# Kernel tuning notes

Hardware: AMD Instinct MI355X
Metric: run time of the kernel (lower is better)

The kernel has to match this reference:

```python
import jax, jax.numpy as jnp
import numpy as np
import math

B, S, D = 2, 1024, 1024
H = 16
HD = D // H
E = 8
DFF = 4096
EPS = 1e-5


def _ln(x, g, b):
    m = jnp.mean(x, axis=-1, keepdims=True)
    v = jnp.mean((x - m) ** 2, axis=-1, keepdims=True)
    return (x - m) / jnp.sqrt(v + EPS) * g + b


def setup_inputs() -> dict:
    key = jax.random.key(0)
    ks = jax.random.split(key, 16)
    s = 0.02
    inp = {
        'src': jax.random.normal(ks[0], (B, S, D), jnp.float32),
        'qw': jax.random.normal(ks[1], (D, D), jnp.float32) * s,
        'kw': jax.random.normal(ks[2], (D, D), jnp.float32) * s,
        'vw': jax.random.normal(ks[3], (D, D), jnp.float32) * s,
        'ow': jax.random.normal(ks[4], (D, D), jnp.float32) * s,
        'gate_w': jax.random.normal(ks[5], (D, D), jnp.float32) * s,
        'gate_b': jax.random.normal(ks[6], (D,), jnp.float32) * s,
        'scale_w': jax.random.normal(ks[7], (H, HD), jnp.float32) * s,
        'n1_g': jnp.ones((D,), jnp.float32),
        'n1_b': jnp.zeros((D,), jnp.float32),
        'n2_g': jnp.ones((D,), jnp.float32),
        'n2_b': jnp.zeros((D,), jnp.float32),
        'moe_gate_w': jax.random.normal(ks[8], (D, E), jnp.float32) * s,
        'moe_gate_b': jnp.zeros((E,), jnp.float32),
        'w1': jax.random.normal(ks[9], (E, D, DFF), jnp.float32) * s,
        'b1': jnp.zeros((E, DFF), jnp.float32),
        'ln_g': jnp.ones((E, DFF), jnp.float32),
        'ln_b': jnp.zeros((E, DFF), jnp.float32),
        'w2': jax.random.normal(ks[10], (E, DFF, D), jnp.float32) * s,
        'b2': jnp.zeros((E, D), jnp.float32),
        'res_scale': jnp.ones((E,), jnp.float32),
    }
    return inp


def _forward(src, qw, kw, vw, ow, gate_w, gate_b, scale_w, n1_g, n1_b, n2_g, n2_b,
             moe_gate_w, moe_gate_b, w1, b1, ln_g, ln_b, w2, b2, res_scale):
    # ---- MemoAttention (non-flash path, eval: no dropout, no mask) ----
    q = (src @ qw).reshape(B, S, H, HD).transpose(0, 2, 1, 3)  # [B,H,S,HD]
    k = (src @ kw).reshape(B, S, H, HD).transpose(0, 2, 1, 3)
    v = (src @ vw).reshape(B, S, H, HD).transpose(0, 2, 1, 3)
    scores = jnp.einsum('bhqd,bhkd->bhqk', q, k) / math.sqrt(HD)
    # dynamic per-(head,query) scale gate
    scale = jax.nn.sigmoid(jnp.einsum('bhsd,hd->bhs', q, scale_w)) * 2.0
    scores = scores * scale[..., None]
    attn = jax.nn.softmax(scores, axis=-1)
    out = jnp.einsum('bhqk,bhkd->bhqd', attn, v)
    out = out.transpose(0, 2, 1, 3).reshape(B, S, D)
    gate = jax.nn.sigmoid(out @ gate_w + gate_b)
    attn_out = (out * gate) @ ow

    x = _ln(src + attn_out, n1_g, n1_b)

    # ---- MoE FFN (top-2 routing; eval: no gate noise; capacity never exceeded) ----
    xf = x.reshape(-1, D)                      # [T, D]
    T = xf.shape[0]
    logits = xf @ moe_gate_w + moe_gate_b      # [T, E]
    top_v, top_i = jax.lax.top_k(logits, 2)
    # NB: original sums BOTH top-k softmax weights per token (== 1.0), and the
    wsum = jnp.sum(jax.nn.softmax(top_v, axis=-1), axis=-1)   # [T] (== 1)
    e_sel = jnp.max(top_i, axis=-1)                           # [T]
    # dense per-expert FFN on all tokens, then per-token select (masked compute)
    h = jnp.einsum('td,edf->etf', xf, w1) + b1[:, None, :]    # [E,T,DFF]
    h = _ln(h, ln_g[:, None, :], ln_b[:, None, :])
    h = jax.nn.gelu(h, approximate=False)                     # torch nn.GELU (erf)
    y = jnp.einsum('etf,efd->etd', h, w2) + b2[:, None, :]    # [E,T,D]
    y = y * res_scale[:, None, None] + xf[None]
    sel = jnp.take_along_axis(y, e_sel[None, :, None], axis=0)[0]  # [T,D]
    moe_out = (sel * wsum[:, None]).reshape(B, S, D)

    return _ln(x + moe_out, n2_g, n2_b)


def reference(src, qw, kw, vw, ow, gate_w, gate_b, scale_w, n1_g, n1_b, n2_g, n2_b,
              moe_gate_w, moe_gate_b, w1, b1, ln_g, ln_b, w2, b2, res_scale):
    return _forward(src, qw, kw, vw, ow, gate_w, gate_b, scale_w, n1_g, n1_b,
                    n2_g, n2_b, moe_gate_w, moe_gate_b, w1, b1, ln_g, ln_b,
                    w2, b2, res_scale)
```

## Files before the change

kernel.cpp:

```cpp
#include <hip/hip_runtime.h>
#include <math.h>

#define TOK    2048
#define DMODEL 1024
#define NHEAD  16
#define HDIM   64
#define NEXP   8
#define DFFN   4096

typedef unsigned short u16;
typedef __attribute__((ext_vector_type(8))) short short8;
typedef __attribute__((ext_vector_type(4))) float floatx4;

__device__ __forceinline__ float sigmoidf_(float x) { return 1.f / (1.f + expf(-x)); }

__device__ __forceinline__ u16 f2bf(float f) {
  union { float f; unsigned u; } v; v.f = f;
  unsigned r = v.u + 0x7FFFu + ((v.u >> 16) & 1u);
  return (u16)(r >> 16);
}
__device__ __forceinline__ float bf2f(u16 h) {
  union { unsigned u; float f; } v; v.u = ((unsigned)h) << 16; return v.f;
}

__device__ __forceinline__ void gload16(const void* g, void* l) {
  __builtin_amdgcn_global_load_lds((const __attribute__((address_space(1))) void*)g,
                                   (__attribute__((address_space(3))) void*)l, 16, 0, 0);
}

__device__ __forceinline__ float blockReduceSum256(float val) {
  __shared__ float ws_[4];
  #pragma unroll
  for (int off = 32; off; off >>= 1) val += __shfl_down(val, off);
  int lane = threadIdx.x & 63, w = threadIdx.x >> 6;
  if (lane == 0) ws_[w] = val;
  __syncthreads();
  float r = ws_[0] + ws_[1] + ws_[2] + ws_[3];
  __syncthreads();
  return r;
}

__global__ __launch_bounds__(256) void split_kernel(
    const float* __restrict__ X, u16* __restrict__ Hi, u16* __restrict__ Lo) {
  const int i = blockIdx.x * 256 + threadIdx.x;
  const float4 v = ((const float4*)X)[i];
  const float f[4] = {v.x, v.y, v.z, v.w};
  union { u16 s[4]; uint2 u; } h, l;
  #pragma unroll
  for (int j = 0; j < 4; ++j) {
    h.s[j] = f2bf(f[j]);
    l.s[j] = f2bf(f[j] - bf2f(h.s[j]));
  }
  ((uint2*)Hi)[i] = h.u;
  ((uint2*)Lo)[i] = l.u;
}

template<bool LO>
__global__ __launch_bounds__(256) void wt_conv_kernel(
    const float* __restrict__ W, u16* __restrict__ Whi, u16* __restrict__ Wlo,
    int K, int N) {
  const size_t z = blockIdx.z;
  W   += z * (size_t)K * N;
  Whi += z * (size_t)K * N;
  if (LO) Wlo += z * (size_t)K * N;
  __shared__ float tile[32][33];
  const int n0 = blockIdx.x * 32, k0 = blockIdx.y * 32;
  const int r = threadIdx.x >> 3, c4 = (threadIdx.x & 7) * 4;
  const float4 v = *(const float4*)&W[(size_t)(k0 + r) * N + n0 + c4];
  tile[r][c4+0] = v.x; tile[r][c4+1] = v.y; tile[r][c4+2] = v.z; tile[r][c4+3] = v.w;
  __syncthreads();
  union { u16 s[4]; uint2 u; } h, l;
  #pragma unroll
  for (int j = 0; j < 4; ++j) {
    const float f = tile[c4 + j][r];
    h.s[j] = f2bf(f);
    if (LO) l.s[j] = f2bf(f - bf2f(h.s[j]));
  }
  *(uint2*)&Whi[(size_t)(n0 + r) * K + k0 + c4] = h.u;
  if (LO) *(uint2*)&Wlo[(size_t)(n0 + r) * K + k0 + c4] = l.u;
}

__global__ __launch_bounds__(256) void wt3_conv_kernel(
    const float* __restrict__ Q, const float* __restrict__ Kw,
    const float* __restrict__ V, u16* __restrict__ Whi, u16* __restrict__ Wlo) {
  const int zz = blockIdx.z >> 5;
  const float* W = (zz == 0) ? Q : (zz == 1) ? Kw : V;
  u16* Whi_ = Whi + (size_t)zz * DMODEL * DMODEL;
  u16* Wlo_ = Wlo + (size_t)zz * DMODEL * DMODEL;
  __shared__ float tile[32][33];
  const int n0 = blockIdx.x * 32, k0 = (blockIdx.z & 31) * 32;
  const int r = threadIdx.x >> 3, c4 = (threadIdx.x & 7) * 4;
  const float4 v = *(const float4*)&W[(size_t)(k0 + r) * DMODEL + n0 + c4];
  tile[r][c4+0] = v.x; tile[r][c4+1] = v.y; tile[r][c4+2] = v.z; tile[r][c4+3] = v.w;
  __syncthreads();
  union { u16 s[4]; uint2 u; } h, l;
  #pragma unroll
  for (int j = 0; j < 4; ++j) {
    const float f = tile[c4 + j][r];
    h.s[j] = f2bf(f);
    l.s[j] = f2bf(f - bf2f(h.s[j]));
  }
  *(uint2*)&Whi_[(size_t)(n0 + r) * DMODEL + k0 + c4] = h.u;
  *(uint2*)&Wlo_[(size_t)(n0 + r) * DMODEL + k0 + c4] = l.u;
}

template<int EPI, int TN>
__global__ __launch_bounds__(256, TN == 64 ? 3 : 2) void gemm_split_kernel(
    const u16* __restrict__ Ahi, const u16* __restrict__ Alo,
    const u16* __restrict__ Whi, const u16* __restrict__ Wlo,
    const float* __restrict__ bias, const float* __restrict__ mul,
    float* __restrict__ Cf, u16* __restrict__ Chi, u16* __restrict__ Clo,
    u16* __restrict__ Vth, u16* __restrict__ Vtl,
    int M, int N, int K) {
  constexpr int NF = TN / 32;
  __shared__ u16 Ah[128*64], Al[128*64], Bh[TN*64], Bl[TN*64];
  const int tid = threadIdx.x;
  const int lane = tid & 63, wave = tid >> 6;
  const int row0 = blockIdx.y * 128, col0 = blockIdx.x * TN;
  const int wm = (wave & 1) * 64, wn = (wave >> 1) * (TN / 2);
  const int mr = tid >> 3;
  const int ksrc = (tid & 7) ^ ((tid >> 3) & 7);
  const floatx4 zero = {0.f, 0.f, 0.f, 0.f};
  floatx4 acc[4][NF];
  #pragma unroll
  for (int i = 0; i < 4; ++i)
    #pragma unroll
    for (int j = 0; j < NF; ++j) acc[i][j] = zero;

  for (int k0 = 0; k0 < K; k0 += 64) {
    __syncthreads();
    #pragma unroll
    for (int p = 0; p < 4; ++p) {
      const size_t ga = (size_t)(row0 + p * 32 + mr) * K + (k0 + ksrc * 8);
      const size_t off = (size_t)(p * 256 + wave * 64) * 16;
      gload16(Ahi + ga, (char*)Ah + off);
      gload16(Alo + ga, (char*)Al + off);
    }
    #pragma unroll
    for (int p = 0; p < NF; ++p) {
      const size_t gb = (size_t)(col0 + p * 32 + mr) * K + (k0 + ksrc * 8);
      const size_t off = (size_t)(p * 256 + wave * 64) * 16;
      gload16(Whi + gb, (char*)Bh + off);
      gload16(Wlo + gb, (char*)Bl + off);
    }
    __syncthreads();
    #pragma unroll
    for (int kk = 0; kk < 2; ++kk) {
      short8 ah[4], al[4], bh[NF], bl[NF];
      #pragma unroll
      for (int i = 0; i < 4; ++i) {
        const int ml = wm + i * 16 + (lane & 15);
        const int cm = (kk * 4 + (lane >> 4)) ^ (ml & 7);
        ah[i] = *(const short8*)&Ah[ml * 64 + cm * 8];
        al[i] = *(const short8*)&Al[ml * 64 + cm * 8];
      }
      #pragma unroll
      for (int j = 0; j < NF; ++j) {
        const int nl = wn + j * 16 + (lane & 15);
        const int cn = (kk * 4 + (lane >> 4)) ^ (nl & 7);
        bh[j] = *(const short8*)&Bh[nl * 64 + cn * 8];
        bl[j] = *(const short8*)&Bl[nl * 64 + cn * 8];
      }
      #pragma unroll
      for (int i = 0; i < 4; ++i)
        #pragma unroll
        for (int j = 0; j < NF; ++j) {
          acc[i][j] = __builtin_amdgcn_mfma_f32_16x16x32_bf16(ah[i], bh[j], acc[i][j], 0, 0, 0);
          acc[i][j] = __builtin_amdgcn_mfma_f32_16x16x32_bf16(al[i], bh[j], acc[i][j], 0, 0, 0);
          acc[i][j] = __builtin_amdgcn_mfma_f32_16x16x32_bf16(ah[i], bl[j], acc[i][j], 0, 0, 0);
        }
    }
  }
  const int cl = lane & 15, quad = lane >> 4;
  if (EPI == 2 && col0 >= 2048) {
    #pragma unroll
    for (int i = 0; i < 4; ++i)
      #pragma unroll
      for (int j = 0; j < NF; ++j) {
        const int dg = col0 + wn + j * 16 + cl - 2048;
        const int bh_ = dg >> 6, d = dg & 63;
        const int row = row0 + wm + i * 16 + quad * 4;
        const int b = row >> 10, t0 = row & 1023;
        union { u16 s[4]; uint2 u; } hh, ll;
        #pragma unroll
        for (int r = 0; r < 4; ++r) {
          const float v = acc[i][j][r];
          hh.s[r] = f2bf(v);
          ll.s[r] = f2bf(v - bf2f(hh.s[r]));
        }
        const size_t base = ((size_t)(b * 16 + bh_) * 64 + d) * 1024 + t0;
        *(uint2*)&Vth[base] = hh.u;
        *(uint2*)&Vtl[base] = ll.u;
      }
    return;
  }
  #pragma unroll
  for (int i = 0; i < 4; ++i)
    #pragma unroll
    for (int j = 0; j < NF; ++j) {
      const int col = col0 + wn + j * 16 + cl;
      #pragma unroll
      for (int r = 0; r < 4; ++r) {
        const int row = row0 + wm + i * 16 + quad * 4 + r;
        const float v = acc[i][j][r];
        if (EPI == 0) {
          Cf[(size_t)row * N + col] = v;
        } else if (EPI == 1) {
          const float s = sigmoidf_(v + bias[col]);
          const float g = s * mul[(size_t)row * N + col];
          const u16 hh = f2bf(g);
          Chi[(size_t)row * N + col] = hh;
          Clo[(size_t)row * N + col] = f2bf(g - bf2f(hh));
        } else {
          const u16 hh = f2bf(v);
          Chi[(size_t)row * N + col] = hh;
          Clo[(size_t)row * N + col] = f2bf(v - bf2f(hh));
        }
      }
    }
}

template<int EPI, int TN>
__global__ __launch_bounds__(256, TN == 64 ? 4 : 3) void gemm_moe_kernel(
    const u16* __restrict__ A, const u16* __restrict__ Wt,
    const float* __restrict__ bias,
    const int* __restrict__ perm, const int* __restrict__ offs,
    const int* __restrict__ counts,
    u16* __restrict__ Hout, float* __restrict__ P0, float* __restrict__ P1,
    int N, int K, int e_base) {
  constexpr int NF = TN / 32;
  const int z = blockIdx.z;
  const int ez = (EPI == 0) ? z : (z & 3);
  const int ks = (EPI == 0) ? 0 : (z >> 2);
  const int e = e_base + ez;
  const int ne = counts[e];
  const int tm = blockIdx.y;
  if (tm * 128 >= ne) return;
  const int kbeg = (EPI == 0) ? 0 : ks * (K >> 1);
  const int kend = (EPI == 0) ? K : kbeg + (K >> 1);
  __shared__ u16 As_[128*64], Bs_[TN*64];
  __shared__ int toks[128];
  const int tid = threadIdx.x;
  if (tid < 128) {
    const int idx = tm * 128 + tid;
    toks[tid] = perm[offs[e] + (idx < ne ? idx : 0)];
  }
  __syncthreads();
  const int lane = tid & 63, wave = tid >> 6;
  const int wm = (wave & 1) * 64, wn = (wave >> 1) * (TN / 2);
  const int mr = tid >> 3;
  const int ksrc = (tid & 7) ^ ((tid >> 3) & 7);
  size_t abase[4];
  #pragma unroll
  for (int p = 0; p < 4; ++p) abase[p] = (size_t)toks[p * 32 + mr] * K;
  const u16* We = Wt + (size_t)ez * N * K;
  const int col0 = blockIdx.x * TN;
  const floatx4 zero = {0.f, 0.f, 0.f, 0.f};
  floatx4 acc[4][NF];
  #pragma unroll
  for (int i = 0; i < 4; ++i)
    #pragma unroll
    for (int j = 0; j < NF; ++j) acc[i][j] = zero;

  for (int k0 = kbeg; k0 < kend; k0 += 64) {
    __syncthreads();
    #pragma unroll
    for (int p = 0; p < 4; ++p) {
      const size_t off = (size_t)(p * 256 + wave * 64) * 16;
      gload16(A + abase[p] + (k0 + ksrc * 8), (char*)As_ + off);
    }
    #pragma unroll
    for (int p = 0; p < NF; ++p) {
      const size_t off = (size_t)(p * 256 + wave * 64) * 16;
      gload16(We + (size_t)(col0 + p * 32 + mr) * K + (k0 + ksrc * 8), (char*)Bs_ + off);
    }
    __syncthreads();
    #pragma unroll
    for (int kk = 0; kk < 2; ++kk) {
      short8 a[4], b[NF];
      #pragma unroll
      for (int i = 0; i < 4; ++i) {
        const int ml = wm + i * 16 + (lane & 15);
        const int cm = (kk * 4 + (lane >> 4)) ^ (ml & 7);
        a[i] = *(const short8*)&As_[ml * 64 + cm * 8];
      }
      #pragma unroll
      for (int j = 0; j < NF; ++j) {
        const int nl = wn + j * 16 + (lane & 15);
        const int cn = (kk * 4 + (lane >> 4)) ^ (nl & 7);
        b[j] = *(const short8*)&Bs_[nl * 64 + cn * 8];
      }
      #pragma unroll
      for (int i = 0; i < 4; ++i)
        #pragma unroll
        for (int j = 0; j < NF; ++j)
          acc[i][j] = __builtin_amdgcn_mfma_f32_16x16x32_bf16(a[i], b[j], acc[i][j], 0, 0, 0);
    }
  }
  const int cl = lane & 15, quad = lane >> 4;
  float* Pp = (EPI == 1) ? (ks ? P1 : P0) : nullptr;
  #pragma unroll
  for (int i = 0; i < 4; ++i)
    #pragma unroll
    for (int j = 0; j < NF; ++j) {
      const int col = col0 + wn + j * 16 + cl;
      #pragma unroll
      for (int r = 0; r < 4; ++r) {
        const int rl = wm + i * 16 + quad * 4 + r;
        if (tm * 128 + rl < ne) {
          const int tok = toks[rl];
          if (EPI == 0)
            Hout[(size_t)tok * N + col] = f2bf(acc[i][j][r] + bias[(size_t)e * N + col]);
          else
            Pp[(size_t)tok * N + col] = acc[i][j][r];
        }
      }
    }
}

__global__ __launch_bounds__(256, 2) void attn_mfma_kernel(
    const u16* __restrict__ QKh, const u16* __restrict__ QKl,
    const u16* __restrict__ Vth, const u16* __restrict__ Vtl,
    const float* __restrict__ scale_w,
    float* __restrict__ AOf, u16* __restrict__ AOh, u16* __restrict__ AOl) {
  const int qt = blockIdx.x, h = blockIdx.y, b = blockIdx.z;
  __shared__ u16 Kh[64*64], Kl[64*64], Vh[64*64], Vl[64*64];
  __shared__ u16 Ph[4][16*72], Pl[4][16*72];
  const int tid = threadIdx.x, lane = tid & 63, wave = tid >> 6;
  const int i15 = lane & 15, quad = lane >> 4;
  const floatx4 zero = {0.f, 0.f, 0.f, 0.f};

  short8 qh[2], ql[2];
  const size_t qrow = ((size_t)b * 1024 + qt * 64 + wave * 16 + i15) * 3072 + h * 64;
  #pragma unroll
  for (int kk = 0; kk < 2; ++kk) {
    qh[kk] = *(const short8*)&QKh[qrow + kk * 32 + quad * 8];
    ql[kk] = *(const short8*)&QKl[qrow + kk * 32 + quad * 8];
  }
  float dot = 0.f;
  #pragma unroll
  for (int kk = 0; kk < 2; ++kk)
    #pragma unroll
    for (int j = 0; j < 8; ++j) {
      const float sw = scale_w[h * 64 + kk * 32 + quad * 8 + j];
      dot += (bf2f((u16)qh[kk][j]) + bf2f((u16)ql[kk][j])) * sw;
    }
  dot += __shfl_xor(dot, 16);
  dot += __shfl_xor(dot, 32);
  const float g = 2.f * sigmoidf_(dot) * 0.125f;
  float stot[4];
  #pragma unroll
  for (int r = 0; r < 4; ++r) stot[r] = __shfl(g, (lane >> 4) * 4 + r);

  float m_r[4], l_r[4];
  floatx4 Of[4];
  #pragma unroll
  for (int r = 0; r < 4; ++r) { m_r[r] = -1e30f; l_r[r] = 0.f; }
  #pragma unroll
  for (int f = 0; f < 4; ++f) Of[f] = zero;
  u16* PhW = Ph[wave];
  u16* PlW = Pl[wave];

  const int sr = tid >> 3, sc = ((tid & 7) ^ ((tid >> 3) & 7)) * 8;
  for (int kt = 0; kt < 16; ++kt) {
    __syncthreads();
    #pragma unroll
    for (int p = 0; p < 2; ++p) {
      const int row = p * 32 + sr;
      const size_t off = (size_t)(p * 256 + wave * 64) * 16;
      const size_t kg = ((size_t)b * 1024 + kt * 64 + row) * 3072 + 1024 + h * 64 + sc;
      gload16(QKh + kg, (char*)Kh + off);
      gload16(QKl + kg, (char*)Kl + off);
      const size_t vg = ((size_t)(b * 16 + h) * 64 + row) * 1024 + kt * 64 + sc;
      gload16(Vth + vg, (char*)Vh + off);
      gload16(Vtl + vg, (char*)Vl + off);
    }
    __syncthreads();
    float pm[4][4];
    #pragma unroll
    for (int jn = 0; jn < 4; ++jn) {
      floatx4 a = zero;
      #pragma unroll
      for (int kk = 0; kk < 2; ++kk) {
        const int n = jn * 16 + i15;
        const int ch = ((kk * 4 + quad) ^ (n & 7)) * 8;
        const short8 bh = *(const short8*)&Kh[n * 64 + ch];
        const short8 bl = *(const short8*)&Kl[n * 64 + ch];
        a = __builtin_amdgcn_mfma_f32_16x16x32_bf16(qh[kk], bh, a, 0, 0, 0);
        a = __builtin_amdgcn_mfma_f32_16x16x32_bf16(ql[kk], bh, a, 0, 0, 0);
        a = __builtin_amdgcn_mfma_f32_16x16x32_bf16(qh[kk], bl, a, 0, 0, 0);
      }
      #pragma unroll
      for (int r = 0; r < 4; ++r) pm[jn][r] = a[r] * stot[r];
    }
    float alpha[4];
    #pragma unroll
    for (int r = 0; r < 4; ++r) {
      float mx = fmaxf(fmaxf(pm[0][r], pm[1][r]), fmaxf(pm[2][r], pm[3][r]));
      mx = fmaxf(mx, __shfl_xor(mx, 1));
      mx = fmaxf(mx, __shfl_xor(mx, 2));
      mx = fmaxf(mx, __shfl_xor(mx, 4));
      mx = fmaxf(mx, __shfl_xor(mx, 8));
      const float mn = fmaxf(m_r[r], mx);
      alpha[r] = expf(m_r[r] - mn);
      m_r[r] = mn;
      float rs = 0.f;
      #pragma unroll
      for (int jn = 0; jn < 4; ++jn) { pm[jn][r] = expf(pm[jn][r] - mn); rs += pm[jn][r]; }
      rs += __shfl_xor(rs, 1);
      rs += __shfl_xor(rs, 2);
      rs += __shfl_xor(rs, 4);
      rs += __shfl_xor(rs, 8);
      l_r[r] = l_r[r] * alpha[r] + rs;
    }
    #pragma unroll
    for (int f = 0; f < 4; ++f)
      #pragma unroll
      for (int r = 0; r < 4; ++r) Of[f][r] *= alpha[r];
    #pragma unroll
    for (int jn = 0; jn < 4; ++jn)
      #pragma unroll
      for (int r = 0; r < 4; ++r) {
        const int a = (quad * 4 + r) * 72 + jn * 16 + i15;
        const u16 hh = f2bf(pm[jn][r]);
        PhW[a] = hh;
        PlW[a] = f2bf(pm[jn][r] - bf2f(hh));
      }
    #pragma unroll
    for (int kk = 0; kk < 2; ++kk) {
      const short8 pah = *(const short8*)&PhW[i15 * 72 + kk * 32 + quad * 8];
      const short8 pal = *(const short8*)&PlW[i15 * 72 + kk * 32 + quad * 8];
      #pragma unroll
      for (int f = 0; f < 4; ++f) {
        const int d = f * 16 + i15;
        const int ch = ((kk * 4 + quad) ^ (d & 7)) * 8;
        const short8 vbh = *(const short8*)&Vh[d * 64 + ch];
        const short8 vbl = *(const short8*)&Vl[d * 64 + ch];
        Of[f] = __builtin_amdgcn_mfma_f32_16x16x32_bf16(pah, vbh, Of[f], 0, 0, 0);
        Of[f] = __builtin_amdgcn_mfma_f32_16x16x32_bf16(pal, vbh, Of[f], 0, 0, 0);
        Of[f] = __builtin_amdgcn_mfma_f32_16x16x32_bf16(pah, vbl, Of[f], 0, 0, 0);
      }
    }
  }
  float inv[4];
  #pragma unroll
  for (int r = 0; r < 4; ++r) inv[r] = 1.f / l_r[r];
  #pragma unroll
  for (int f = 0; f < 4; ++f)
    #pragma unroll
    for (int r = 0; r < 4; ++r) {
      const size_t row = (size_t)b * 1024 + qt * 64 + wave * 16 + quad * 4 + r;
      const int col = h * 64 + f * 16 + i15;
      const float val = Of[f][r] * inv[r];
      AOf[row * 1024 + col] = val;
      const u16 hh = f2bf(val);
      AOh[row * 1024 + col] = hh;
      AOl[row * 1024 + col] = f2bf(val - bf2f(hh));
    }
}

template<bool BF>
__global__ __launch_bounds__(256) void ln_add_kernel(
    const float* __restrict__ A, const float* __restrict__ Bp,
    const float* __restrict__ g, const float* __restrict__ beta,
    float* __restrict__ outf, u16* __restrict__ outh) {
  int t = blockIdx.x, tid = threadIdx.x;
  const float* a = A + (size_t)t * DMODEL;
  const float* b = Bp + (size_t)t * DMODEL;
  float v[4]; float s = 0.f;
  #pragma unroll
  for (int i = 0; i < 4; ++i) { int d = tid + i*256; v[i] = a[d] + b[d]; s += v[i]; }
  s = blockReduceSum256(s);
  float mean = s * (1.f/1024.f);
  float q = 0.f;
  #pragma unroll
  for (int i = 0; i < 4; ++i) { float df = v[i]-mean; q += df*df; }
  q = blockReduceSum256(q);
  float rstd = rsqrtf(q*(1.f/1024.f) + 1e-5f);
  #pragma unroll
  for (int i = 0; i < 4; ++i) {
    int d = tid + i*256;
    float val = (v[i]-mean)*rstd*g[d] + beta[d];
    outf[(size_t)t*DMODEL + d] = val;
    if (BF) outh[(size_t)t*DMODEL + d] = f2bf(val);
  }
}

__global__ __launch_bounds__(256) void ln_final_kernel(
    const float* __restrict__ X, const float* __restrict__ P0,
    const float* __restrict__ P1, const float* __restrict__ B2,
    const float* __restrict__ rsv, const int* __restrict__ e_sel,
    const float* __restrict__ g, const float* __restrict__ beta,
    float* __restrict__ out) {
  int t = blockIdx.x, tid = threadIdx.x;
  const int e = e_sel[t];
  const float rse = rsv[e];
  const float* b2e = B2 + (size_t)e * DMODEL;
  float v[4]; float s = 0.f;
  #pragma unroll
  for (int i = 0; i < 4; ++i) {
    int d = tid + i*256;
    const size_t idx = (size_t)t * DMODEL + d;
    const float xv = X[idx];
    const float yv = (P0[idx] + P1[idx] + b2e[d]) * rse + xv;
    v[i] = xv + yv;
    s += v[i];
  }
  s = blockReduceSum256(s);
  float mean = s * (1.f/1024.f);
  float q = 0.f;
  #pragma unroll
  for (int i = 0; i < 4; ++i) { float df = v[i]-mean; q += df*df; }
  q = blockReduceSum256(q);
  float rstd = rsqrtf(q*(1.f/1024.f) + 1e-5f);
  #pragma unroll
  for (int i = 0; i < 4; ++i) {
    int d = tid + i*256;
    out[(size_t)t*DMODEL + d] = (v[i]-mean)*rstd*g[d] + beta[d];
  }
}

__global__ __launch_bounds__(256) void moe_gate_kernel(
    const float* __restrict__ X, const float* __restrict__ gw,
    const float* __restrict__ gb, int* __restrict__ e_sel) {
  int wave = threadIdx.x >> 6, lane = threadIdx.x & 63;
  int token = blockIdx.x * 4 + wave;
  const float* x = X + (size_t)token * DMODEL;
  float acc[NEXP] = {};
  for (int d = lane; d < DMODEL; d += 64) {
    float xv = x[d];
    const float* gr = gw + (size_t)d * NEXP;
    #pragma unroll
    for (int e = 0; e < NEXP; ++e) acc[e] += xv * gr[e];
  }
  #pragma unroll
  for (int e = 0; e < NEXP; ++e) {
    #pragma unroll
    for (int off = 32; off; off >>= 1) acc[e] += __shfl_down(acc[e], off);
  }
  if (lane == 0) {
    float lg[NEXP];
    #pragma unroll
    for (int e = 0; e < NEXP; ++e) lg[e] = acc[e] + gb[e];
    int i1 = 0;
    for (int e = 1; e < NEXP; ++e) if (lg[e] > lg[i1]) i1 = e;
    int i2 = -1;
    for (int e = 0; e < NEXP; ++e) {
      if (e == i1) continue;
      if (i2 < 0 || lg[e] > lg[i2]) i2 = e;
    }
    e_sel[token] = (i1 > i2) ? i1 : i2;
  }
}

__global__ __launch_bounds__(256) void moe_group_kernel(
    const int* __restrict__ e_sel, int* __restrict__ perm,
    int* __restrict__ g_offs, int* __restrict__ g_counts) {
  __shared__ int cnt[NEXP], offs[NEXP], cur[NEXP];
  int tid = threadIdx.x;
  if (tid < NEXP) cnt[tid] = 0;
  __syncthreads();
  for (int t = tid; t < TOK; t += 256) atomicAdd(&cnt[e_sel[t]], 1);
  __syncthreads();
  if (tid == 0) {
    int run = 0;
    for (int e = 0; e < NEXP; ++e) { offs[e] = run; cur[e] = run; run += cnt[e]; }
  }
  __syncthreads();
  if (tid < NEXP) { g_offs[tid] = offs[tid]; g_counts[tid] = cnt[tid]; }
  for (int t = tid; t < TOK; t += 256) {
    int pos = atomicAdd(&cur[e_sel[t]], 1);
    perm[pos] = t;
  }
}

__global__ __launch_bounds__(256) void moe_ln_gelu_kernel(
    u16* __restrict__ H, const float* __restrict__ ln_g,
    const float* __restrict__ ln_b, const int* __restrict__ e_sel) {
  int t = blockIdx.x, tid = threadIdx.x;
  int e = e_sel[t];
  u16* h = H + (size_t)t * DFFN;
  float v[16]; float s = 0.f;
  #pragma unroll
  for (int i = 0; i < 16; ++i) { v[i] = bf2f(h[tid + i*256]); s += v[i]; }
  s = blockReduceSum256(s);
  float mean = s * (1.f/4096.f);
  float q = 0.f;
  #pragma unroll
  for (int i = 0; i < 16; ++i) { float df = v[i]-mean; q += df*df; }
  q = blockReduceSum256(q);
  float rstd = rsqrtf(q*(1.f/4096.f) + 1e-5f);
  const float* gg = ln_g + (size_t)e * DFFN;
  const float* bb = ln_b + (size_t)e * DFFN;
  #pragma unroll
  for (int i = 0; i < 16; ++i) {
    int d = tid + i*256;
    float x = (v[i]-mean)*rstd*gg[d] + bb[d];
    h[d] = f2bf(0.5f * x * (1.f + erff(x * 0.7071067811865475f)));
  }
}

extern "C" void kernel_launch(void* const* d_in, const int* in_sizes, int n_in,
                              void* d_out, int out_size, void* d_ws, size_t ws_size,
                              hipStream_t stream) {
  (void)in_sizes; (void)n_in; (void)out_size; (void)ws_size;
  const float* src    = (const float*)d_in[0];
  const float* qw     = (const float*)d_in[1];
  const float* kw     = (const float*)d_in[2];
  const float* vw     = (const float*)d_in[3];
  const float* ow     = (const float*)d_in[4];
  const float* gate_w = (const float*)d_in[5];
  const float* gate_b = (const float*)d_in[6];
  const float* scale_w= (const float*)d_in[7];
  const float* n1_g   = (const float*)d_in[8];
  const float* n1_b   = (const float*)d_in[9];
  const float* n2_g   = (const float*)d_in[10];
  const float* n2_b   = (const float*)d_in[11];
  const float* mgw    = (const float*)d_in[12];
  const float* mgb    = (const float*)d_in[13];
  const float* w1     = (const float*)d_in[14];
  const float* b1     = (const float*)d_in[15];
  const float* ln_g   = (const float*)d_in[16];
  const float* ln_b   = (const float*)d_in[17];
  const float* w2     = (const float*)d_in[18];
  const float* b2     = (const float*)d_in[19];
  const float* rs     = (const float*)d_in[20];

  char* ws = (char*)d_ws;
  const size_t MB = 1024 * 1024;
  u16*   qkv_hi = (u16*)(ws + 0*MB);
  u16*   qkv_lo = (u16*)(ws + 12*MB);
  u16*   Wt3_hi = (u16*)(ws + 24*MB);
  u16*   Wt3_lo = (u16*)(ws + 30*MB);
  u16*   Vt_hi  = (u16*)(ws + 36*MB);
  u16*   Vt_lo  = (u16*)(ws + 40*MB);
  u16*   src_hi = (u16*)(ws + 44*MB);
  u16*   src_lo = (u16*)(ws + 48*MB);
  float* ao     = (float*)(ws + 44*MB);
  u16*   ao_hi  = (u16*)(ws + 52*MB);
  u16*   ao_lo  = (u16*)(ws + 56*MB);
  u16*   gb_hi  = (u16*)(ws + 60*MB);
  u16*   gb_lo  = (u16*)(ws + 64*MB);
  float* proj   = (float*)(ws + 0*MB);
  float* x      = (float*)(ws + 8*MB);
  u16*   x_hi   = (u16*)(ws + 16*MB);
  u16*   WtA    = (u16*)(ws + 24*MB);
  u16*   h      = (u16*)(ws + 56*MB);
  float* p0     = (float*)(ws + 0*MB);
  float* p1     = (float*)(ws + 72*MB);
  int*   e_sel  = (int*)(ws + 80*MB);
  int*   perm   = e_sel + TOK;
  int*   offs   = perm + TOK;
  int*   cnts   = offs + NEXP;

  dim3 blk(256);
  split_kernel<<<2048, blk, 0, stream>>>(src, src_hi, src_lo);

  wt3_conv_kernel<<<dim3(32,1,96), blk, 0, stream>>>(qw, kw, vw, Wt3_hi, Wt3_lo);
  gemm_split_kernel<2,128><<<dim3(24,16), blk, 0, stream>>>(src_hi, src_lo, Wt3_hi, Wt3_lo,
      nullptr, nullptr, nullptr, qkv_hi, qkv_lo, Vt_hi, Vt_lo, TOK, 3072, DMODEL);

  attn_mfma_kernel<<<dim3(16, NHEAD, 2), blk, 0, stream>>>(
      qkv_hi, qkv_lo, Vt_hi, Vt_lo, scale_w, ao, ao_hi, ao_lo);

  wt_conv_kernel<true><<<dim3(32,32,1), blk, 0, stream>>>(gate_w, Wt3_hi, Wt3_lo, DMODEL, DMODEL);
  gemm_split_kernel<1,64><<<dim3(16,16), blk, 0, stream>>>(ao_hi, ao_lo, Wt3_hi, Wt3_lo,
      gate_b, ao, nullptr, gb_hi, gb_lo, nullptr, nullptr, TOK, DMODEL, DMODEL);
  wt_conv_kernel<true><<<dim3(32,32,1), blk, 0, stream>>>(ow, Wt3_hi, Wt3_lo, DMODEL, DMODEL);
  gemm_split_kernel<0,64><<<dim3(16,16), blk, 0, stream>>>(gb_hi, gb_lo, Wt3_hi, Wt3_lo,
      nullptr, nullptr, proj, nullptr, nullptr, nullptr, nullptr, TOK, DMODEL, DMODEL);

  ln_add_kernel<true><<<TOK, blk, 0, stream>>>(src, proj, n1_g, n1_b, x, x_hi);

  moe_gate_kernel<<<TOK/4, blk, 0, stream>>>(x, mgw, mgb, e_sel);
  moe_group_kernel<<<1, blk, 0, stream>>>(e_sel, perm, offs, cnts);

  for (int c = 0; c < 2; ++c) {
    wt_conv_kernel<false><<<dim3(DFFN/32, DMODEL/32, 4), blk, 0, stream>>>(
        w1 + (size_t)c*4*DMODEL*DFFN, WtA, nullptr, DMODEL, DFFN);
    gemm_moe_kernel<0,128><<<dim3(DFFN/128, 16, 4), blk, 0, stream>>>(
        x_hi, WtA, b1, perm, offs, cnts, h, nullptr, nullptr, DFFN, DMODEL, c*4);
  }
  moe_ln_gelu_kernel<<<TOK, blk, 0, stream>>>(h, ln_g, ln_b, e_sel);
  for (int c = 0; c < 2; ++c) {
    wt_conv_kernel<false><<<dim3(DMODEL/32, DFFN/32, 4), blk, 0, stream>>>(
        w2 + (size_t)c*4*DFFN*DMODEL, WtA, nullptr, DFFN, DMODEL);
    gemm_moe_kernel<1,64><<<dim3(DMODEL/64, 16, 8), blk, 0, stream>>>(
        h, WtA, nullptr, perm, offs, cnts, nullptr, p0, p1, DMODEL, DFFN, c*4);
  }
  ln_final_kernel<<<TOK, blk, 0, stream>>>(x, p0, p1, b2, rs, e_sel, n2_g, n2_b, (float*)d_out);
}
```

Baseline: 726.2 us.

## Widen attention blocks to 128 queries, vectorize LN kernels, use fast exp

The attention kernel now runs 512 threads per block covering 128 queries, so each K/V tile load is shared by twice as many query rows. Its per-wave P staging buffer is halved by writing and consuming one 32-key chunk at a time. Softmax and sigmoid switch to __expf, and the final residual+LN and the expert LN+GELU kernels use float4/uint2 vectorized accesses. The QKV GEMM moves to a 64-wide tile with twice as many blocks. Costs are fewer attention blocks in flight (256) and slightly less accurate exponentials.

Result: no change. 713.7 us (-1.7%).

```diff
diff --git a/kernel.cpp b/kernel.cpp
--- a/kernel.cpp
+++ b/kernel.cpp
@@ -12,7 +12,7 @@
 typedef __attribute__((ext_vector_type(8))) short short8;
 typedef __attribute__((ext_vector_type(4))) float floatx4;
 
-__device__ __forceinline__ float sigmoidf_(float x) { return 1.f / (1.f + expf(-x)); }
+__device__ __forceinline__ float sigmoidf_(float x) { return 1.f / (1.f + __expf(-x)); }
 
 __device__ __forceinline__ u16 f2bf(float f) {
   union { float f; unsigned u; } v; v.f = f;
@@ -318,20 +318,20 @@
     }
 }
 
-__global__ __launch_bounds__(256, 2) void attn_mfma_kernel(
+__global__ __launch_bounds__(512, 2) void attn_mfma_kernel(
     const u16* __restrict__ QKh, const u16* __restrict__ QKl,
     const u16* __restrict__ Vth, const u16* __restrict__ Vtl,
     const float* __restrict__ scale_w,
     float* __restrict__ AOf, u16* __restrict__ AOh, u16* __restrict__ AOl) {
   const int qt = blockIdx.x, h = blockIdx.y, b = blockIdx.z;
   __shared__ u16 Kh[64*64], Kl[64*64], Vh[64*64], Vl[64*64];
-  __shared__ u16 Ph[4][16*72], Pl[4][16*72];
+  __shared__ u16 Ph[8][16*40], Pl[8][16*40];
   const int tid = threadIdx.x, lane = tid & 63, wave = tid >> 6;
   const int i15 = lane & 15, quad = lane >> 4;
   const floatx4 zero = {0.f, 0.f, 0.f, 0.f};
 
   short8 qh[2], ql[2];
-  const size_t qrow = ((size_t)b * 1024 + qt * 64 + wave * 16 + i15) * 3072 + h * 64;
+  const size_t qrow = ((size_t)b * 1024 + qt * 128 + wave * 16 + i15) * 3072 + h * 64;
   #pragma unroll
   for (int kk = 0; kk < 2; ++kk) {
     qh[kk] = *(const short8*)&QKh[qrow + kk * 32 + quad * 8];
@@ -361,17 +361,16 @@
   u16* PhW = Ph[wave];
   u16* PlW = Pl[wave];
 
-  const int sr = tid >> 3, sc = ((tid & 7) ^ ((tid >> 3) & 7)) * 8;
+  const int sr = tid >> 3;
+  const int sc = ((tid & 7) ^ (sr & 7)) * 8;
   for (int kt = 0; kt < 16; ++kt) {
     __syncthreads();
-    #pragma unroll
-    for (int p = 0; p < 2; ++p) {
-      const int row = p * 32 + sr;
-      const size_t off = (size_t)(p * 256 + wave * 64) * 16;
-      const size_t kg = ((size_t)b * 1024 + kt * 64 + row) * 3072 + 1024 + h * 64 + sc;
+    {
+      const size_t off = (size_t)wave * 1024;
+      const size_t kg = ((size_t)b * 1024 + kt * 64 + sr) * 3072 + 1024 + h * 64 + sc;
       gload16(QKh + kg, (char*)Kh + off);
       gload16(QKl + kg, (char*)Kl + off);
-      const size_t vg = ((size_t)(b * 16 + h) * 64 + row) * 1024 + kt * 64 + sc;
+      const size_t vg = ((size_t)(b * 16 + h) * 64 + sr) * 1024 + kt * 64 + sc;
       gload16(Vth + vg, (char*)Vh + off);
       gload16(Vtl + vg, (char*)Vl + off);
     }
@@ -402,11 +401,11 @@
       mx = fmaxf(mx, __shfl_xor(mx, 4));
       mx = fmaxf(mx, __shfl_xor(mx, 8));
       const float mn = fmaxf(m_r[r], mx);
-      alpha[r] = expf(m_r[r] - mn);
+      alpha[r] = __expf(m_r[r] - mn);
       m_r[r] = mn;
       float rs = 0.f;
       #pragma unroll
-      for (int jn = 0; jn < 4; ++jn) { pm[jn][r] = expf(pm[jn][r] - mn); rs += pm[jn][r]; }
+      for (int jn = 0; jn < 4; ++jn) { pm[jn][r] = __expf(pm[jn][r] - mn); rs += pm[jn][r]; }
       rs += __shfl_xor(rs, 1);
       rs += __shfl_xor(rs, 2);
       rs += __shfl_xor(rs, 4);
@@ -418,18 +417,20 @@
       #pragma unroll
       for (int r = 0; r < 4; ++r) Of[f][r] *= alpha[r];
     #pragma unroll
-    for (int jn = 0; jn < 4; ++jn)
-      #pragma unroll
-      for (int r = 0; r < 4; ++r) {
-        const int a = (quad * 4 + r) * 72 + jn * 16 + i15;
-        const u16 hh = f2bf(pm[jn][r]);
-        PhW[a] = hh;
-        PlW[a] = f2bf(pm[jn][r] - bf2f(hh));
-      }
-    #pragma unroll
     for (int kk = 0; kk < 2; ++kk) {
-      const short8 pah = *(const short8*)&PhW[i15 * 72 + kk * 32 + quad * 8];
-      const short8 pal = *(const short8*)&PlW[i15 * 72 + kk * 32 + quad * 8];
+      #pragma unroll
+      for (int jj = 0; jj < 2; ++jj) {
+        const int jn = kk * 2 + jj;
+        #pragma unroll
+        for (int r = 0; r < 4; ++r) {
+          const int a = (quad * 4 + r) * 40 + jj * 16 + i15;
+          const u16 hh = f2bf(pm[jn][r]);
+          PhW[a] = hh;
+          PlW[a] = f2bf(pm[jn][r] - bf2f(hh));
+        }
+      }
+      const short8 pah = *(const short8*)&PhW[i15 * 40 + quad * 8];
+      const short8 pal = *(const short8*)&PlW[i15 * 40 + quad * 8];
       #pragma unroll
       for (int f = 0; f < 4; ++f) {
         const int d = f * 16 + i15;
@@ -449,7 +450,7 @@
   for (int f = 0; f < 4; ++f)
     #pragma unroll
     for (int r = 0; r < 4; ++r) {
-      const size_t row = (size_t)b * 1024 + qt * 64 + wave * 16 + quad * 4 + r;
+      const size_t row = (size_t)b * 1024 + qt * 128 + wave * 16 + quad * 4 + r;
       const int col = h * 64 + f * 16 + i15;
       const float val = Of[f][r] * inv[r];
       AOf[row * 1024 + col] = val;
@@ -496,16 +497,18 @@
   const int e = e_sel[t];
   const float rse = rsv[e];
   const float* b2e = B2 + (size_t)e * DMODEL;
+  const int d0 = tid * 4;
+  const size_t base = (size_t)t * DMODEL + d0;
+  const float4 xv = *(const float4*)&X[base];
+  const float4 p0v = *(const float4*)&P0[base];
+  const float4 p1v = *(const float4*)&P1[base];
+  const float4 bv = *(const float4*)&b2e[d0];
   float v[4]; float s = 0.f;
-  #pragma unroll
-  for (int i = 0; i < 4; ++i) {
-    int d = tid + i*256;
-    const size_t idx = (size_t)t * DMODEL + d;
-    const float xv = X[idx];
-    const float yv = (P0[idx] + P1[idx] + b2e[d]) * rse + xv;
-    v[i] = xv + yv;
-    s += v[i];
-  }
+  v[0] = 2.f*xv.x + (p0v.x + p1v.x + bv.x) * rse;
+  v[1] = 2.f*xv.y + (p0v.y + p1v.y + bv.y) * rse;
+  v[2] = 2.f*xv.z + (p0v.z + p1v.z + bv.z) * rse;
+  v[3] = 2.f*xv.w + (p0v.w + p1v.w + bv.w) * rse;
+  s = v[0] + v[1] + v[2] + v[3];
   s = blockReduceSum256(s);
   float mean = s * (1.f/1024.f);
   float q = 0.f;
@@ -513,11 +516,14 @@
   for (int i = 0; i < 4; ++i) { float df = v[i]-mean; q += df*df; }
   q = blockReduceSum256(q);
   float rstd = rsqrtf(q*(1.f/1024.f) + 1e-5f);
-  #pragma unroll
-  for (int i = 0; i < 4; ++i) {
-    int d = tid + i*256;
-    out[(size_t)t*DMODEL + d] = (v[i]-mean)*rstd*g[d] + beta[d];
-  }
+  const float4 g4 = *(const float4*)&g[d0];
+  const float4 be4 = *(const float4*)&beta[d0];
+  float4 o;
+  o.x = (v[0]-mean)*rstd*g4.x + be4.x;
+  o.y = (v[1]-mean)*rstd*g4.y + be4.y;
+  o.z = (v[2]-mean)*rstd*g4.z + be4.z;
+  o.w = (v[3]-mean)*rstd*g4.w + be4.w;
+  *(float4*)&out[base] = o;
 }
 
 __global__ __launch_bounds__(256) void moe_gate_kernel(
@@ -579,10 +585,16 @@
     const float* __restrict__ ln_b, const int* __restrict__ e_sel) {
   int t = blockIdx.x, tid = threadIdx.x;
   int e = e_sel[t];
-  u16* h = H + (size_t)t * DFFN;
+  u16* hp = H + (size_t)t * DFFN;
   float v[16]; float s = 0.f;
   #pragma unroll
-  for (int i = 0; i < 16; ++i) { v[i] = bf2f(h[tid + i*256]); s += v[i]; }
+  for (int i = 0; i < 4; ++i) {
+    const int d = i * 1024 + tid * 4;
+    union { uint2 u; u16 q[4]; } hv;
+    hv.u = *(const uint2*)&hp[d];
+    #pragma unroll
+    for (int j = 0; j < 4; ++j) { v[i*4+j] = bf2f(hv.q[j]); s += v[i*4+j]; }
+  }
   s = blockReduceSum256(s);
   float mean = s * (1.f/4096.f);
   float q = 0.f;
@@ -593,10 +605,19 @@
   const float* gg = ln_g + (size_t)e * DFFN;
   const float* bb = ln_b + (size_t)e * DFFN;
   #pragma unroll
-  for (int i = 0; i < 16; ++i) {
-    int d = tid + i*256;
-    float x = (v[i]-mean)*rstd*gg[d] + bb[d];
-    h[d] = f2bf(0.5f * x * (1.f + erff(x * 0.7071067811865475f)));
+  for (int i = 0; i < 4; ++i) {
+    const int d = i * 1024 + tid * 4;
+    const float4 g4 = *(const float4*)&gg[d];
+    const float4 b4 = *(const float4*)&bb[d];
+    const float gf[4] = {g4.x, g4.y, g4.z, g4.w};
+    const float bf[4] = {b4.x, b4.y, b4.z, b4.w};
+    union { uint2 u; u16 q[4]; } ov;
+    #pragma unroll
+    for (int j = 0; j < 4; ++j) {
+      float xx = (v[i*4+j]-mean)*rstd*gf[j] + bf[j];
+      ov.q[j] = f2bf(0.5f * xx * (1.f + erff(xx * 0.7071067811865475f)));
+    }
+    *(uint2*)&hp[d] = ov.u;
   }
 }
 
@@ -657,10 +678,10 @@
   split_kernel<<<2048, blk, 0, stream>>>(src, src_hi, src_lo);
 
   wt3_conv_kernel<<<dim3(32,1,96), blk, 0, stream>>>(qw, kw, vw, Wt3_hi, Wt3_lo);
-  gemm_split_kernel<2,128><<<dim3(24,16), blk, 0, stream>>>(src_hi, src_lo, Wt3_hi, Wt3_lo,
+  gemm_split_kernel<2,64><<<dim3(48,16), blk, 0, stream>>>(src_hi, src_lo, Wt3_hi, Wt3_lo,
       nullptr, nullptr, nullptr, qkv_hi, qkv_lo, Vt_hi, Vt_lo, TOK, 3072, DMODEL);
 
-  attn_mfma_kernel<<<dim3(16, NHEAD, 2), blk, 0, stream>>>(
+  attn_mfma_kernel<<<dim3(8, NHEAD, 2), dim3(512), 0, stream>>>(
       qkv_hi, qkv_lo, Vt_hi, Vt_lo, scale_w, ao, ao_hi, ao_lo);
 
   wt_conv_kernel<true><<<dim3(32,32,1), blk, 0, stream>>>(gate_w, Wt3_hi, Wt3_lo, DMODEL, DMODEL);
```
